# Kernel optimization log

Measured on AMD Instinct MI355X. Metric: run time of the kernel, lower is better.

## Reference

```python
import jax, jax.numpy as jnp
import numpy as np

B, T, C, H = 4, 2048, 1024, 16
D = C // H  # head_dim = 64


def setup_inputs() -> dict:
    key = jax.random.key(0)
    k1, k2, k3 = jax.random.split(key, 3)
    x = jax.random.normal(k1, (B, T, C), dtype=jnp.float32)
    w_attn = jax.random.normal(k2, (C, 3 * C), dtype=jnp.float32) * (1.0 / np.sqrt(C))
    b_attn = jnp.zeros((3 * C,), dtype=jnp.float32)
    w_proj = jax.random.normal(k3, (C, C), dtype=jnp.float32) * (1.0 / np.sqrt(C))
    b_proj = jnp.zeros((C,), dtype=jnp.float32)
    return {"x": x, "w_attn": w_attn, "b_attn": b_attn, "w_proj": w_proj, "b_proj": b_proj}


def reference(x, w_attn, b_attn, w_proj, b_proj):
    Bx, Tx, Cx = x.shape
    qkv = x @ w_attn + b_attn                      # (B, T, 3C)
    q, k, v = jnp.split(qkv, 3, axis=2)
    # (B, T, C) -> (B, H, T, D)
    q = q.reshape(Bx, Tx, H, D).transpose(0, 2, 1, 3)
    k = k.reshape(Bx, Tx, H, D).transpose(0, 2, 1, 3)
    v = v.reshape(Bx, Tx, H, D).transpose(0, 2, 1, 3)
    scores = jnp.einsum('bhqd,bhkd->bhqk', q, k) / jnp.sqrt(jnp.float32(D))
    causal = jnp.tril(jnp.ones((Tx, Tx), dtype=bool))
    scores = jnp.where(causal[None, None], scores, jnp.float32(-jnp.inf))
    probs = jax.nn.softmax(scores, axis=-1)
    out = jnp.einsum('bhqk,bhkd->bhqd', probs, v)  # (B, H, T, D)
    out = out.transpose(0, 2, 1, 3).reshape(Bx, Tx, Cx)
    return out @ w_proj + b_proj
```

## Files before the change

### kernel.cpp

```cpp
#include <hip/hip_runtime.h>

#define AS1 __attribute__((address_space(1)))
#define AS3 __attribute__((address_space(3)))

using bf16x8  = __attribute__((ext_vector_type(8))) __bf16;
using floatx4 = __attribute__((ext_vector_type(4))) float;

#define SCQ 0.18033688f

__device__ inline ushort f2b(float f) {
    __bf16 h = (__bf16)f;
    return __builtin_bit_cast(ushort, h);
}

__device__ inline float fexp2(float x) {
    float r;
    asm("v_exp_f32 %0, %1" : "=v"(r) : "v"(x));
    return r;
}

__device__ inline unsigned cvtpk_bf16(float lo, float hi) {
    unsigned r;
    asm("v_cvt_pk_bf16_f32 %0, %1, %2" : "=v"(r) : "v"(lo), "v"(hi));
    return r;
}
__device__ inline void plswap32(unsigned& a, unsigned& b) {
    asm("v_permlane32_swap_b32 %0, %1" : "+v"(a), "+v"(b));
}
__device__ inline void plswap16(unsigned& a, unsigned& b) {
    asm("v_permlane16_swap_b32 %0, %1" : "+v"(a), "+v"(b));
}

__device__ inline bf16x8 pack_swap(floatx4 ej0, floatx4 ej1) {
    unsigned x0 = cvtpk_bf16(ej0[0], ej0[1]);
    unsigned x1 = cvtpk_bf16(ej0[2], ej0[3]);
    unsigned y0 = cvtpk_bf16(ej1[0], ej1[1]);
    unsigned y1 = cvtpk_bf16(ej1[2], ej1[3]);
    plswap32(x0, y0); plswap16(x0, y0);
    plswap32(x1, y1); plswap16(x1, y1);
    union { unsigned u[4]; bf16x8 v; } ua;
    ua.u[0] = x0; ua.u[1] = x1; ua.u[2] = y0; ua.u[3] = y1;
    return ua.v;
}

__global__ void k_prep(const float* __restrict__ x, ushort* __restrict__ xb,
                       const float* __restrict__ wa, ushort* __restrict__ waT,
                       const float* __restrict__ wp, ushort* __restrict__ wpT)
{
    __shared__ float tile[32][33];
    int blk = blockIdx.x;
    if (blk < 8192) {
        int i = (blk * 256 + threadIdx.x) * 4;
        float4 v = *(const float4*)(x + i);
        ushort4 o;
        o.x = f2b(v.x); o.y = f2b(v.y); o.z = f2b(v.z); o.w = f2b(v.w);
        *(ushort4*)(xb + i) = o;
        return;
    }
    const float* in; ushort* out; int R, Ncol, bx, by; float scale; int scale_cols;
    if (blk < 11264) {
        int idx = blk - 8192;
        in = wa; out = waT; R = 1024; Ncol = 3072;
        bx = idx % 96; by = idx / 96; scale = SCQ; scale_cols = 1024;
    } else {
        int idx = blk - 11264;
        in = wp; out = wpT; R = 1024; Ncol = 1024;
        bx = idx % 32; by = idx / 32; scale = 1.0f; scale_cols = 0;
    }
    int tx = threadIdx.x & 31, ty = threadIdx.x >> 5;
    int c0 = bx * 32, r0 = by * 32;
    for (int i = 0; i < 32; i += 8)
        tile[ty + i][tx] = in[(size_t)(r0 + ty + i) * Ncol + c0 + tx];
    __syncthreads();
    for (int i = 0; i < 32; i += 8) {
        int n = c0 + ty + i;
        float v = tile[tx][ty + i];
        if (n < scale_cols) v *= scale;
        out[(size_t)n * R + r0 + tx] = f2b(v);
    }
}

__global__ __launch_bounds__(256, 2) void k_gemm_bt(
    const ushort* __restrict__ A, const ushort* __restrict__ Bt,
    const float* __restrict__ bias, float* __restrict__ outv,
    int M, int N, int K)
{
    __shared__ __align__(16) ushort As[128 * 64];
    __shared__ __align__(16) ushort Bs[128 * 64];
    int tid = threadIdx.x;
    int m0 = blockIdx.y * 128, n0 = blockIdx.x * 128;
    int lane = tid & 63;
    int wm = (tid >> 7) * 64;
    int wn = ((tid >> 6) & 1) * 64;
    int lr = lane & 15, quad = lane >> 4;

    floatx4 acc[4][4] = {};
    const ushort* ags[4]; const ushort* bgs[4]; int sdst[4];
    #pragma unroll
    for (int it = 0; it < 4; ++it) {
        int slot = tid + 256 * it;
        int row = slot >> 3, ch = slot & 7;
        ags[it] = A  + (size_t)(m0 + row) * K + ch * 8;
        bgs[it] = Bt + (size_t)(n0 + row) * K + ch * 8;
        sdst[it] = slot * 8;
    }

    for (int kt = 0; kt < K; kt += 64) {
        #pragma unroll
        for (int it = 0; it < 4; ++it) {
            __builtin_amdgcn_global_load_lds((const AS1 unsigned int*)(ags[it] + kt),
                                             (AS3 unsigned int*)&As[sdst[it]], 16, 0, 0);
            __builtin_amdgcn_global_load_lds((const AS1 unsigned int*)(bgs[it] + kt),
                                             (AS3 unsigned int*)&Bs[sdst[it]], 16, 0, 0);
        }
        asm volatile("s_waitcnt vmcnt(0)" ::: "memory");
        __syncthreads();
        bf16x8 af[4][2], bf[4][2];
        #pragma unroll
        for (int i = 0; i < 4; ++i) {
            af[i][0] = *(const bf16x8*)&As[(wm + 16 * i + lr) * 64 + quad * 8];
            af[i][1] = *(const bf16x8*)&As[(wm + 16 * i + lr) * 64 + 32 + quad * 8];
        }
        #pragma unroll
        for (int j = 0; j < 4; ++j) {
            bf[j][0] = *(const bf16x8*)&Bs[(wn + 16 * j + lr) * 64 + quad * 8];
            bf[j][1] = *(const bf16x8*)&Bs[(wn + 16 * j + lr) * 64 + 32 + quad * 8];
        }
        #pragma unroll
        for (int i = 0; i < 4; ++i)
            #pragma unroll
            for (int j = 0; j < 4; ++j) {
                acc[i][j] = __builtin_amdgcn_mfma_f32_16x16x32_bf16(af[i][0], bf[j][0], acc[i][j], 0, 0, 0);
                acc[i][j] = __builtin_amdgcn_mfma_f32_16x16x32_bf16(af[i][1], bf[j][1], acc[i][j], 0, 0, 0);
            }
        __syncthreads();
    }

    #pragma unroll
    for (int j = 0; j < 4; ++j) {
        int col = n0 + wn + 16 * j + lr;
        float bv = bias[col];
        #pragma unroll
        for (int i = 0; i < 4; ++i) {
            int row = m0 + wm + 16 * i + quad * 4;
            #pragma unroll
            for (int r = 0; r < 4; ++r)
                outv[(size_t)(row + r) * N + col] = acc[i][j][r] + bv;
        }
    }
}

__global__ __launch_bounds__(256, 2) void k_gemm_qkv(
    const ushort* __restrict__ A, const ushort* __restrict__ Bt,
    const float* __restrict__ bias, ushort* __restrict__ qkv, ushort* __restrict__ vt)
{
    constexpr int K = 1024;
    __shared__ __align__(16) ushort As[128 * 64];
    __shared__ __align__(16) ushort Bs[128 * 64];
    int tid = threadIdx.x;
    int m0 = blockIdx.y * 128, n0 = blockIdx.x * 128;
    int lane = tid & 63;
    int wm = (tid >> 7) * 64;
    int wn = ((tid >> 6) & 1) * 64;
    int lr = lane & 15, quad = lane >> 4;

    floatx4 acc[4][4] = {};
    const ushort* ags[4]; const ushort* bgs[4]; int sdst[4];
    #pragma unroll
    for (int it = 0; it < 4; ++it) {
        int slot = tid + 256 * it;
        int row = slot >> 3, ch = slot & 7;
        ags[it] = A  + (size_t)(m0 + row) * K + ch * 8;
        bgs[it] = Bt + (size_t)(n0 + row) * K + ch * 8;
        sdst[it] = slot * 8;
    }

    for (int kt = 0; kt < K; kt += 64) {
        #pragma unroll
        for (int it = 0; it < 4; ++it) {
            __builtin_amdgcn_global_load_lds((const AS1 unsigned int*)(ags[it] + kt),
                                             (AS3 unsigned int*)&As[sdst[it]], 16, 0, 0);
            __builtin_amdgcn_global_load_lds((const AS1 unsigned int*)(bgs[it] + kt),
                                             (AS3 unsigned int*)&Bs[sdst[it]], 16, 0, 0);
        }
        asm volatile("s_waitcnt vmcnt(0)" ::: "memory");
        __syncthreads();
        bf16x8 af[4][2], bf[4][2];
        #pragma unroll
        for (int i = 0; i < 4; ++i) {
            af[i][0] = *(const bf16x8*)&As[(wm + 16 * i + lr) * 64 + quad * 8];
            af[i][1] = *(const bf16x8*)&As[(wm + 16 * i + lr) * 64 + 32 + quad * 8];
        }
        #pragma unroll
        for (int j = 0; j < 4; ++j) {
            bf[j][0] = *(const bf16x8*)&Bs[(wn + 16 * j + lr) * 64 + quad * 8];
            bf[j][1] = *(const bf16x8*)&Bs[(wn + 16 * j + lr) * 64 + 32 + quad * 8];
        }
        #pragma unroll
        for (int i = 0; i < 4; ++i)
            #pragma unroll
            for (int j = 0; j < 4; ++j) {
                acc[i][j] = __builtin_amdgcn_mfma_f32_16x16x32_bf16(af[i][0], bf[j][0], acc[i][j], 0, 0, 0);
                acc[i][j] = __builtin_amdgcn_mfma_f32_16x16x32_bf16(af[i][1], bf[j][1], acc[i][j], 0, 0, 0);
            }
        __syncthreads();
    }

    int bb = m0 >> 11;
    #pragma unroll
    for (int j = 0; j < 4; ++j) {
        int col = n0 + wn + 16 * j + lr;
        float bv = bias[col];
        if (col < 1024) bv *= SCQ;
        if (col < 2048) {
            #pragma unroll
            for (int i = 0; i < 4; ++i) {
                int row = m0 + wm + 16 * i + quad * 4;
                #pragma unroll
                for (int r = 0; r < 4; ++r)
                    qkv[(size_t)(row + r) * 2048 + col] = f2b(acc[i][j][r] + bv);
            }
        } else {
            int h = (col - 2048) >> 6, d = (col - 2048) & 63;
            ushort* vbase = vt + ((size_t)(bb * 16 + h) * 64 + d) * 2048;
            #pragma unroll
            for (int i = 0; i < 4; ++i) {
                int t0 = (m0 + wm + 16 * i + quad * 4) & 2047;
                ushort4 pk;
                ((ushort*)&pk)[0] = f2b(acc[i][j][0] + bv);
                ((ushort*)&pk)[1] = f2b(acc[i][j][1] + bv);
                ((ushort*)&pk)[2] = f2b(acc[i][j][2] + bv);
                ((ushort*)&pk)[3] = f2b(acc[i][j][3] + bv);
                *(ushort4*)&vbase[t0] = pk;
            }
        }
    }
}

__global__ __launch_bounds__(512, 4) void k_attn(const ushort* __restrict__ qkv,
                                                 const ushort* __restrict__ vt,
                                                 ushort* __restrict__ out)
{
    constexpr int T = 2048, SQK = 2048, C = 1024;
    __shared__ __align__(16) ushort Ks[4][64 * 64];
    __shared__ __align__(16) ushort Vs[4][64 * 64];
    int tid = threadIdx.x;
    int lane = tid & 63, wave = tid >> 6;
    int lr = lane & 15, quad = lane >> 4, lk = quad * 8;
    int bh = blockIdx.y;
    int b = bh >> 4, h = bh & 15;
    size_t base = (size_t)b * T * SQK;
    const ushort* kg0 = qkv + base + 1024 + h * 64;
    const ushort* vg0 = vt + (size_t)bh * 64 * 2048;

    int srow = tid >> 3;
    int sg   = (tid & 7) ^ (srow & 7);
    int sdst = tid * 8;
    const ushort* kgs = kg0 + (size_t)srow * SQK + sg * 8;
    const ushort* vgs = vg0 + (size_t)srow * 2048 + sg * 8;

    bf16x8 ones;
    #pragma unroll
    for (int i = 0; i < 8; ++i) ones[i] = (__bf16)1.0f;
    int c0 = (quad ^ (lr & 7)) * 8;
    int c1 = ((4 + quad) ^ (lr & 7)) * 8;

    int qts[2] = { (int)blockIdx.x, 15 - (int)blockIdx.x };
    for (int ti = 0; ti < 2; ++ti) {
        int qt = qts[ti];
        int qrow = qt * 128 + wave * 16;
        int kt_d = qrow >> 6;
        const ushort* qp = qkv + base + (size_t)(qrow + lr) * SQK + h * 64;
        bf16x8 aq0 = *(const bf16x8*)(qp + lk);
        bf16x8 aq1 = *(const bf16x8*)(qp + 32 + lk);
        floatx4 o[4] = {};
        floatx4 lacc = {};
        int ktmax = 2 * qt + 1;

        __syncthreads();

        __builtin_amdgcn_global_load_lds((const AS1 unsigned int*)kgs,
                                         (AS3 unsigned int*)&Ks[0][sdst], 16, 0, 0);
        __builtin_amdgcn_global_load_lds((const AS1 unsigned int*)vgs,
                                         (AS3 unsigned int*)&Vs[0][sdst], 16, 0, 0);
        if (ktmax >= 1) {
            __builtin_amdgcn_global_load_lds((const AS1 unsigned int*)(kgs + (size_t)64 * SQK),
                                             (AS3 unsigned int*)&Ks[1][sdst], 16, 0, 0);
            __builtin_amdgcn_global_load_lds((const AS1 unsigned int*)(vgs + 64),
                                             (AS3 unsigned int*)&Vs[1][sdst], 16, 0, 0);
        }
        if (ktmax >= 2) {
            __builtin_amdgcn_global_load_lds((const AS1 unsigned int*)(kgs + (size_t)2 * 64 * SQK),
                                             (AS3 unsigned int*)&Ks[2][sdst], 16, 0, 0);
            __builtin_amdgcn_global_load_lds((const AS1 unsigned int*)(vgs + 2 * 64),
                                             (AS3 unsigned int*)&Vs[2][sdst], 16, 0, 0);
        }

        for (int kt = 0; kt <= ktmax; ++kt) {
            __syncthreads();
            if (kt + 3 <= ktmax) {
                int bidx = (kt + 3) & 3;
                __builtin_amdgcn_global_load_lds((const AS1 unsigned int*)(kgs + (size_t)(kt + 3) * 64 * SQK),
                                                 (AS3 unsigned int*)&Ks[bidx][sdst], 16, 0, 0);
                __builtin_amdgcn_global_load_lds((const AS1 unsigned int*)(vgs + (kt + 3) * 64),
                                                 (AS3 unsigned int*)&Vs[bidx][sdst], 16, 0, 0);
                asm volatile("s_waitcnt vmcnt(6)" ::: "memory");
            } else if (kt + 2 <= ktmax) {
                asm volatile("s_waitcnt vmcnt(4)" ::: "memory");
            } else if (kt + 1 <= ktmax) {
                asm volatile("s_waitcnt vmcnt(2)" ::: "memory");
            } else {
                asm volatile("s_waitcnt vmcnt(0)" ::: "memory");
            }
            __syncthreads();

            if (kt > kt_d) continue;
            const ushort* Kb = Ks[kt & 3];
            const ushort* Vb = Vs[kt & 3];

            floatx4 s[4];
            __builtin_amdgcn_s_setprio(1);
            #pragma unroll
            for (int j = 0; j < 4; ++j) {
                const ushort* kr = &Kb[(16 * j + lr) * 64];
                bf16x8 bk0 = *(const bf16x8*)(kr + c0);
                bf16x8 bk1 = *(const bf16x8*)(kr + c1);
                floatx4 z = {};
                s[j] = __builtin_amdgcn_mfma_f32_16x16x32_bf16(bk0, aq0, z, 0, 0, 0);
                s[j] = __builtin_amdgcn_mfma_f32_16x16x32_bf16(bk1, aq1, s[j], 0, 0, 0);
            }
            __builtin_amdgcn_s_setprio(0);

            floatx4 e[4];
            if (kt == kt_d) {
                int qa = qrow + lr;
                #pragma unroll
                for (int j = 0; j < 4; ++j)
                    #pragma unroll
                    for (int r = 0; r < 4; ++r)
                        e[j][r] = ((kt * 64 + 16 * j + quad * 4 + r) > qa) ? 0.f : fexp2(s[j][r]);
            } else {
                #pragma unroll
                for (int j = 0; j < 4; ++j)
                    #pragma unroll
                    for (int r = 0; r < 4; ++r)
                        e[j][r] = fexp2(s[j][r]);
            }
            bf16x8 ap0 = pack_swap(e[0], e[1]);
            bf16x8 ap1 = pack_swap(e[2], e[3]);

            __builtin_amdgcn_s_setprio(1);
            lacc = __builtin_amdgcn_mfma_f32_16x16x32_bf16(ap0, ones, lacc, 0, 0, 0);
            lacc = __builtin_amdgcn_mfma_f32_16x16x32_bf16(ap1, ones, lacc, 0, 0, 0);
            #pragma unroll
            for (int jd = 0; jd < 4; ++jd) {
                const ushort* vr = &Vb[(16 * jd + lr) * 64];
                bf16x8 bv0 = *(const bf16x8*)(vr + c0);
                bf16x8 bv1 = *(const bf16x8*)(vr + c1);
                o[jd] = __builtin_amdgcn_mfma_f32_16x16x32_bf16(ap0, bv0, o[jd], 0, 0, 0);
                o[jd] = __builtin_amdgcn_mfma_f32_16x16x32_bf16(ap1, bv1, o[jd], 0, 0, 0);
            }
            __builtin_amdgcn_s_setprio(0);
        }

        #pragma unroll
        for (int r = 0; r < 4; ++r) {
            float inv = 1.0f / lacc[r];
            int row = b * T + qrow + quad * 4 + r;
            #pragma unroll
            for (int jd = 0; jd < 4; ++jd)
                out[(size_t)row * C + h * 64 + 16 * jd + lr] = f2b(o[jd][r] * inv);
        }
    }
}

extern "C" void kernel_launch(void* const* d_in, const int* in_sizes, int n_in,
                              void* d_out, int out_size, void* d_ws, size_t ws_size,
                              hipStream_t stream) {
    const float* x      = (const float*)d_in[0];
    const float* w_attn = (const float*)d_in[1];
    const float* b_attn = (const float*)d_in[2];
    const float* w_proj = (const float*)d_in[3];
    const float* b_proj = (const float*)d_in[4];
    float* out = (float*)d_out;

    constexpr int Bb = 4, T = 2048, C = 1024;
    constexpr int M = Bb * T;

    ushort* xb  = (ushort*)d_ws;
    ushort* waT = xb  + (size_t)M * C;
    ushort* wpT = waT + (size_t)3 * C * C;
    ushort* qkv = wpT + (size_t)C * C;
    ushort* vt  = qkv + (size_t)M * 2 * C;
    ushort* ao  = vt  + (size_t)64 * 64 * T;

    k_prep<<<12288, 256, 0, stream>>>(x, xb, w_attn, waT, w_proj, wpT);
    k_gemm_qkv<<<dim3(3 * C / 128, M / 128), 256, 0, stream>>>(xb, waT, b_attn, qkv, vt);
    k_attn<<<dim3(8, Bb * 16), 512, 0, stream>>>(qkv, vt, ao);
    k_gemm_bt<<<dim3(C / 128, M / 128), 256, 0, stream>>>(ao, wpT, b_proj, out, M, C, C);
}
```

Baseline: 244.1 us.

## Share K/V tiles across paired causal query tiles; add XCD-aware block swizzle

The attention kernel now handles its two query tiles (qt and 15-qt) in a single pass over the K/V stream. Each K/V tile loaded into LDS is used by both queries, so the earlier tiles are no longer loaded twice. Block indices are also remapped so that blocks with the same batch-head are spread in a chosen order. Both GEMM kernels get an XCD swizzle of their block index to improve L2 locality across chiplets. The fused pass holds two sets of accumulators, which raises register pressure and may lower occupancy. The host launch grid must match the new 8-wide linearization, and that part is not shown.

```diff
diff --git a/kernel.cpp b/kernel.cpp
--- a/kernel.cpp
+++ b/kernel.cpp
@@ -80,6 +80,13 @@
     }
 }
 
+__device__ inline void xcd_swizzle(int& bx, int& by) {
+    int gx = gridDim.x, lin = blockIdx.x + gx * blockIdx.y;
+    int nwg = gx * gridDim.y;
+    int swz = (lin & 7) * (nwg >> 3) + (lin >> 3);
+    bx = swz % gx; by = swz / gx;
+}
+
 __global__ __launch_bounds__(256, 2) void k_gemm_bt(
     const ushort* __restrict__ A, const ushort* __restrict__ Bt,
     const float* __restrict__ bias, float* __restrict__ outv,
@@ -88,7 +95,8 @@
     __shared__ __align__(16) ushort As[128 * 64];
     __shared__ __align__(16) ushort Bs[128 * 64];
     int tid = threadIdx.x;
-    int m0 = blockIdx.y * 128, n0 = blockIdx.x * 128;
+    int bxs, bys; xcd_swizzle(bxs, bys);
+    int m0 = bys * 128, n0 = bxs * 128;
     int lane = tid & 63;
     int wm = (tid >> 7) * 64;
     int wn = ((tid >> 6) & 1) * 64;
@@ -158,7 +166,8 @@
     __shared__ __align__(16) ushort As[128 * 64];
     __shared__ __align__(16) ushort Bs[128 * 64];
     int tid = threadIdx.x;
-    int m0 = blockIdx.y * 128, n0 = blockIdx.x * 128;
+    int bxs, bys; xcd_swizzle(bxs, bys);
+    int m0 = bys * 128, n0 = bxs * 128;
     int lane = tid & 63;
     int wm = (tid >> 7) * 64;
     int wn = ((tid >> 6) & 1) * 64;
@@ -235,6 +244,55 @@
             }
         }
     }
+}
+
+__device__ __forceinline__ void attn_tile(
+    const ushort* __restrict__ Kb, const ushort* __restrict__ Vb,
+    bf16x8 aq0, bf16x8 aq1, bf16x8 ones,
+    floatx4 (&o)[4], floatx4& lacc,
+    int kt, int ktd, int qrow, int lr, int quad, int c0, int c1)
+{
+    floatx4 s[4];
+    __builtin_amdgcn_s_setprio(1);
+    #pragma unroll
+    for (int j = 0; j < 4; ++j) {
+        const ushort* kr = &Kb[(16 * j + lr) * 64];
+        bf16x8 bk0 = *(const bf16x8*)(kr + c0);
+        bf16x8 bk1 = *(const bf16x8*)(kr + c1);
+        floatx4 z = {};
+        s[j] = __builtin_amdgcn_mfma_f32_16x16x32_bf16(bk0, aq0, z, 0, 0, 0);
+        s[j] = __builtin_amdgcn_mfma_f32_16x16x32_bf16(bk1, aq1, s[j], 0, 0, 0);
+    }
+    __builtin_amdgcn_s_setprio(0);
+    floatx4 e[4];
+    if (kt == ktd) {
+        int qa = qrow + lr;
+        #pragma unroll
+        for (int j = 0; j < 4; ++j)
+            #pragma unroll
+            for (int r = 0; r < 4; ++r)
+                e[j][r] = ((kt * 64 + 16 * j + quad * 4 + r) > qa) ? 0.f : fexp2(s[j][r]);
+    } else {
+        #pragma unroll
+        for (int j = 0; j < 4; ++j)
+            #pragma unroll
+            for (int r = 0; r < 4; ++r)
+                e[j][r] = fexp2(s[j][r]);
+    }
+    bf16x8 ap0 = pack_swap(e[0], e[1]);
+    bf16x8 ap1 = pack_swap(e[2], e[3]);
+    __builtin_amdgcn_s_setprio(1);
+    lacc = __builtin_amdgcn_mfma_f32_16x16x32_bf16(ap0, ones, lacc, 0, 0, 0);
+    lacc = __builtin_amdgcn_mfma_f32_16x16x32_bf16(ap1, ones, lacc, 0, 0, 0);
+    #pragma unroll
+    for (int jd = 0; jd < 4; ++jd) {
+        const ushort* vr = &Vb[(16 * jd + lr) * 64];
+        bf16x8 bv0 = *(const bf16x8*)(vr + c0);
+        bf16x8 bv1 = *(const bf16x8*)(vr + c1);
+        o[jd] = __builtin_amdgcn_mfma_f32_16x16x32_bf16(ap0, bv0, o[jd], 0, 0, 0);
+        o[jd] = __builtin_amdgcn_mfma_f32_16x16x32_bf16(ap1, bv1, o[jd], 0, 0, 0);
+    }
+    __builtin_amdgcn_s_setprio(0);
 }
 
 __global__ __launch_bounds__(512, 4) void k_attn(const ushort* __restrict__ qkv,
@@ -247,7 +305,10 @@
     int tid = threadIdx.x;
     int lane = tid & 63, wave = tid >> 6;
     int lr = lane & 15, quad = lane >> 4, lk = quad * 8;
-    int bh = blockIdx.y;
+
+    int lin = blockIdx.x + 8 * blockIdx.y;
+    int qt  = lin >> 6;
+    int bh  = lin & 63;
     int b = bh >> 4, h = bh & 15;
     size_t base = (size_t)b * T * SQK;
     const ushort* kg0 = qkv + base + 1024 + h * 64;
@@ -265,111 +326,64 @@
     int c0 = (quad ^ (lr & 7)) * 8;
     int c1 = ((4 + quad) ^ (lr & 7)) * 8;
 
-    int qts[2] = { (int)blockIdx.x, 15 - (int)blockIdx.x };
-    for (int ti = 0; ti < 2; ++ti) {
-        int qt = qts[ti];
-        int qrow = qt * 128 + wave * 16;
-        int kt_d = qrow >> 6;
-        const ushort* qp = qkv + base + (size_t)(qrow + lr) * SQK + h * 64;
-        bf16x8 aq0 = *(const bf16x8*)(qp + lk);
-        bf16x8 aq1 = *(const bf16x8*)(qp + 32 + lk);
-        floatx4 o[4] = {};
-        floatx4 lacc = {};
-        int ktmax = 2 * qt + 1;
-
-        __syncthreads();
-
-        __builtin_amdgcn_global_load_lds((const AS1 unsigned int*)kgs,
-                                         (AS3 unsigned int*)&Ks[0][sdst], 16, 0, 0);
-        __builtin_amdgcn_global_load_lds((const AS1 unsigned int*)vgs,
-                                         (AS3 unsigned int*)&Vs[0][sdst], 16, 0, 0);
-        if (ktmax >= 1) {
-            __builtin_amdgcn_global_load_lds((const AS1 unsigned int*)(kgs + (size_t)64 * SQK),
-                                             (AS3 unsigned int*)&Ks[1][sdst], 16, 0, 0);
-            __builtin_amdgcn_global_load_lds((const AS1 unsigned int*)(vgs + 64),
-                                             (AS3 unsigned int*)&Vs[1][sdst], 16, 0, 0);
-        }
-        if (ktmax >= 2) {
-            __builtin_amdgcn_global_load_lds((const AS1 unsigned int*)(kgs + (size_t)2 * 64 * SQK),
-                                             (AS3 unsigned int*)&Ks[2][sdst], 16, 0, 0);
-            __builtin_amdgcn_global_load_lds((const AS1 unsigned int*)(vgs + 2 * 64),
-                                             (AS3 unsigned int*)&Vs[2][sdst], 16, 0, 0);
-        }
-
-        for (int kt = 0; kt <= ktmax; ++kt) {
-            __syncthreads();
-            if (kt + 3 <= ktmax) {
-                int bidx = (kt + 3) & 3;
-                __builtin_amdgcn_global_load_lds((const AS1 unsigned int*)(kgs + (size_t)(kt + 3) * 64 * SQK),
-                                                 (AS3 unsigned int*)&Ks[bidx][sdst], 16, 0, 0);
-                __builtin_amdgcn_global_load_lds((const AS1 unsigned int*)(vgs + (kt + 3) * 64),
-                                                 (AS3 unsigned int*)&Vs[bidx][sdst], 16, 0, 0);
-                asm volatile("s_waitcnt vmcnt(6)" ::: "memory");
-            } else if (kt + 2 <= ktmax) {
-                asm volatile("s_waitcnt vmcnt(4)" ::: "memory");
-            } else if (kt + 1 <= ktmax) {
-                asm volatile("s_waitcnt vmcnt(2)" ::: "memory");
-            } else {
-                asm volatile("s_waitcnt vmcnt(0)" ::: "memory");
-            }
-            __syncthreads();
-
-            if (kt > kt_d) continue;
-            const ushort* Kb = Ks[kt & 3];
-            const ushort* Vb = Vs[kt & 3];
-
-            floatx4 s[4];
-            __builtin_amdgcn_s_setprio(1);
-            #pragma unroll
-            for (int j = 0; j < 4; ++j) {
-                const ushort* kr = &Kb[(16 * j + lr) * 64];
-                bf16x8 bk0 = *(const bf16x8*)(kr + c0);
-                bf16x8 bk1 = *(const bf16x8*)(kr + c1);
-                floatx4 z = {};
-                s[j] = __builtin_amdgcn_mfma_f32_16x16x32_bf16(bk0, aq0, z, 0, 0, 0);
-                s[j] = __builtin_amdgcn_mfma_f32_16x16x32_bf16(bk1, aq1, s[j], 0, 0, 0);
-            }
-            __builtin_amdgcn_s_setprio(0);
-
-            floatx4 e[4];
-            if (kt == kt_d) {
-                int qa = qrow + lr;
-                #pragma unroll
-                for (int j = 0; j < 4; ++j)
-                    #pragma unroll
-                    for (int r = 0; r < 4; ++r)
-                        e[j][r] = ((kt * 64 + 16 * j + quad * 4 + r) > qa) ? 0.f : fexp2(s[j][r]);
-            } else {
-                #pragma unroll
-                for (int j = 0; j < 4; ++j)
-                    #pragma unroll
-                    for (int r = 0; r < 4; ++r)
-                        e[j][r] = fexp2(s[j][r]);
-            }
-            bf16x8 ap0 = pack_swap(e[0], e[1]);
-            bf16x8 ap1 = pack_swap(e[2], e[3]);
-
-            __builtin_amdgcn_s_setprio(1);
-            lacc = __builtin_amdgcn_mfma_f32_16x16x32_bf16(ap0, ones, lacc, 0, 0, 0);
-            lacc = __builtin_amdgcn_mfma_f32_16x16x32_bf16(ap1, ones, lacc, 0, 0, 0);
-            #pragma unroll
-            for (int jd = 0; jd < 4; ++jd) {
-                const ushort* vr = &Vb[(16 * jd + lr) * 64];
-                bf16x8 bv0 = *(const bf16x8*)(vr + c0);
-                bf16x8 bv1 = *(const bf16x8*)(vr + c1);
-                o[jd] = __builtin_amdgcn_mfma_f32_16x16x32_bf16(ap0, bv0, o[jd], 0, 0, 0);
-                o[jd] = __builtin_amdgcn_mfma_f32_16x16x32_bf16(ap1, bv1, o[jd], 0, 0, 0);
-            }
-            __builtin_amdgcn_s_setprio(0);
-        }
-
-        #pragma unroll
-        for (int r = 0; r < 4; ++r) {
-            float inv = 1.0f / lacc[r];
-            int row = b * T + qrow + quad * 4 + r;
-            #pragma unroll
-            for (int jd = 0; jd < 4; ++jd)
-                out[(size_t)row * C + h * 64 + 16 * jd + lr] = f2b(o[jd][r] * inv);
+    int qtA = qt, qtB = 15 - qt;
+    int qrowA = qtA * 128 + wave * 16;
+    int qrowB = qtB * 128 + wave * 16;
+    int ktdA = qrowA >> 6, ktdB = qrowB >> 6;
+    const ushort* qpA = qkv + base + (size_t)(qrowA + lr) * SQK + h * 64;
+    const ushort* qpB = qkv + base + (size_t)(qrowB + lr) * SQK + h * 64;
+    bf16x8 aqA0 = *(const bf16x8*)(qpA + lk);
+    bf16x8 aqA1 = *(const bf16x8*)(qpA + 32 + lk);
+    bf16x8 aqB0 = *(const bf16x8*)(qpB + lk);
+    bf16x8 aqB1 = *(const bf16x8*)(qpB + 32 + lk);
+    floatx4 oA[4] = {}, oB[4] = {};
+    floatx4 laccA = {}, laccB = {};
+    int ktmax = 2 * qtB + 1;
+
+    #pragma unroll
+    for (int p = 0; p < 3; ++p) {
+        __builtin_amdgcn_global_load_lds((const AS1 unsigned int*)(kgs + (size_t)p * 64 * SQK),
+                                         (AS3 unsigned int*)&Ks[p][sdst], 16, 0, 0);
+        __builtin_amdgcn_global_load_lds((const AS1 unsigned int*)(vgs + p * 64),
+                                         (AS3 unsigned int*)&Vs[p][sdst], 16, 0, 0);
+    }
+
+    for (int kt = 0; kt <= ktmax; ++kt) {
+        __syncthreads();
+        if (kt + 3 <= ktmax) {
+            int bidx = (kt + 3) & 3;
+            __builtin_amdgcn_global_load_lds((const AS1 unsigned int*)(kgs + (size_t)(kt + 3) * 64 * SQK),
+                                             (AS3 unsigned int*)&Ks[bidx][sdst], 16, 0, 0);
+            __builtin_amdgcn_global_load_lds((const AS1 unsigned int*)(vgs + (kt + 3) * 64),
+                                             (AS3 unsigned int*)&Vs[bidx][sdst], 16, 0, 0);
+            asm volatile("s_waitcnt vmcnt(6)" ::: "memory");
+        } else if (kt + 2 <= ktmax) {
+            asm volatile("s_waitcnt vmcnt(4)" ::: "memory");
+        } else if (kt + 1 <= ktmax) {
+            asm volatile("s_waitcnt vmcnt(2)" ::: "memory");
+        } else {
+            asm volatile("s_waitcnt vmcnt(0)" ::: "memory");
+        }
+        __syncthreads();
+
+        const ushort* Kb = Ks[kt & 3];
+        const ushort* Vb = Vs[kt & 3];
+        if (kt <= ktdB)
+            attn_tile(Kb, Vb, aqB0, aqB1, ones, oB, laccB, kt, ktdB, qrowB, lr, quad, c0, c1);
+        if (kt <= ktdA)
+            attn_tile(Kb, Vb, aqA0, aqA1, ones, oA, laccA, kt, ktdA, qrowA, lr, quad, c0, c1);
+    }
+
+    #pragma unroll
+    for (int r = 0; r < 4; ++r) {
+        float invA = 1.0f / laccA[r];
+        float invB = 1.0f / laccB[r];
+        int rowA = b * T + qrowA + quad * 4 + r;
+        int rowB = b * T + qrowB + quad * 4 + r;
+        #pragma unroll
+        for (int jd = 0; jd < 4; ++jd) {
+            out[(size_t)rowA * C + h * 64 + 16 * jd + lr] = f2b(oA[jd][r] * invA);
+            out[(size_t)rowB * C + h * 64 + 16 * jd + lr] = f2b(oB[jd][r] * invB);
         }
     }
 }
```

Result: faster. 235.6 us (-3.5%).
